# Performance work log

Hardware: AMD Instinct MI355X
Metric: run time of the kernel (lower is better)

The kernel has to match this reference:

```python
import jax, jax.numpy as jnp
import numpy as np

EPS = 0.5
GAM1 = 1.0
GAM2 = 1.0
GAM3 = 1.0
NUM_CLASS = 10


def _logdet(M):
    return jnp.linalg.slogdet(M)[1]


def _discrimn_loss(Z):
    # Z: [n, d] sample-major (original code operates on Z.T of shape (d, n))
    n, d = Z.shape
    scalar = d / (n * EPS)
    I = jnp.eye(d, dtype=Z.dtype)
    return _logdet(I + scalar * (Z.T @ Z)) / 2.0


def _class_grams(Z, Pi):
    # Pi: [n, C] one-hot (float). G[c] = sum_{i in class c} z_i z_i^T  -> [C, d, d]
    return jnp.einsum('nc,nd,ne->cde', Pi, Z, Z)


def _compress_losses(G, counts, d, n):
    # per-class logdet(I + (d/(trPi*eps)) * Gram_c), trPi = count + 1e-8
    C = G.shape[0]
    trPi = counts + 1e-8
    scal = d / (trPi * EPS)                      # [C]
    I = jnp.eye(d, dtype=G.dtype)
    M = I[None, :, :] + scal[:, None, None] * G  # [C, d, d]
    lds = jax.vmap(_logdet)(M)                   # [C]
    lds = jnp.where(counts == 0, 1.0, lds)       # original uses 1.0 for empty class
    scalars = trPi / (2.0 * n)
    return lds, scalars


def setup_inputs() -> dict:
    key = jax.random.key(0)
    k1, k2, k3 = jax.random.split(key, 3)
    n, d = 8192, 512
    Z = jax.random.normal(k1, (n, d), dtype=jnp.float32)
    Z_bar = jax.random.normal(k2, (n, d), dtype=jnp.float32)
    real_label = jax.random.randint(k3, (n,), 0, NUM_CLASS, dtype=jnp.int64 if jax.config.jax_enable_x64 else jnp.int32)
    return {"Z": Z, "Z_bar": Z_bar, "real_label": real_label,
            "ith_inner_loop": 0, "num_inner_loop": 2}


def reference(Z, Z_bar, real_label, ith_inner_loop, num_inner_loop):
    n, d = Z.shape
    Pi = jax.nn.one_hot(real_label, NUM_CLASS, dtype=Z.dtype)  # [n, C]
    counts = Pi.sum(axis=0)                                    # [C]

    # deltaR(Z) and deltaR(Z_bar)
    z_disc = _discrimn_loss(Z)
    zb_disc = _discrimn_loss(Z_bar)
    Gz = _class_grams(Z, Pi)
    Gzb = _class_grams(Z_bar, Pi)
    z_lds, z_scalars = _compress_losses(Gz, counts, d, n)
    zb_lds, zb_scalars = _compress_losses(Gzb, counts, d, n)
    z_comp = jnp.sum(z_scalars * z_lds)
    zb_comp = jnp.sum(zb_scalars * zb_lds)
    z_total = -(z_disc - z_comp)
    zbar_total = -(zb_disc - zb_comp)

    # cross term: for each class j, discrimn loss of cat(Z[y==j], Z_bar[y==j])
    # Gram of concatenation = Gz[j] + Gzb[j]; n_j = 2*count_j
    nj = 2.0 * counts
    scal = d / (nj * EPS)                                       # [C]
    I = jnp.eye(d, dtype=Z.dtype)
    Mcross = I[None, :, :] + scal[:, None, None] * (Gz + Gzb)
    cross_lds = jax.vmap(_logdet)(Mcross) / 2.0
    itemRzjzjbar = jnp.sum(cross_lds)

    errD_ = (GAM1 * (z_disc - z_comp)
             + GAM2 * (zb_disc - zb_comp)
             + GAM3 * (itemRzjzjbar - 0.25 * jnp.sum(z_lds) - 0.25 * jnp.sum(zb_lds)))
    errD = -errD_
    term3 = -itemRzjzjbar + 0.25 * jnp.sum(z_lds) + 0.25 * jnp.sum(zb_lds)
    return (errD, z_total, zbar_total, term3)
```

## Files before the change

### kernel.cpp

```cpp
#include <hip/hip_runtime.h>
#include <math.h>

#define D     512
#define NCLS  10
#define GKB   32
#define NB    16
#define CHOLT 512
#define SSTR  20

__global__ __launch_bounds__(1024) void meta_kernel(const int* __restrict__ labels, int n,
                                                    int* __restrict__ counts,
                                                    int* __restrict__ offsets,
                                                    int* __restrict__ perm) {
    __shared__ int sc[NCLS], scur[NCLS], soff[NCLS + 1];
    int t = threadIdx.x;
    if (t < NCLS) { sc[t] = 0; scur[t] = 0; }
    __syncthreads();
    for (int i = t; i < n; i += 1024) atomicAdd(&sc[labels[i]], 1);
    __syncthreads();
    if (t == 0) {
        int a = 0;
        for (int c = 0; c < NCLS; ++c) { soff[c] = a; a += sc[c]; }
        soff[NCLS] = a;
    }
    __syncthreads();
    for (int i = t; i < n; i += 1024) {
        int l = labels[i];
        int pos = soff[l] + atomicAdd(&scur[l], 1);
        perm[pos] = i;
    }
    if (t < NCLS) { counts[t] = sc[t]; offsets[t] = soff[t]; }
}

__global__ __launch_bounds__(256) void gram_kernel(const float* __restrict__ Z,
                                                   const float* __restrict__ Zb,
                                                   const int* __restrict__ offsets,
                                                   const int* __restrict__ counts,
                                                   const int* __restrict__ perm,
                                                   float* __restrict__ Gz,
                                                   float* __restrict__ Gzb) {
    const int job = blockIdx.y;
    const int tensor = job / NCLS;
    const int c = job % NCLS;
    const float* __restrict__ A = tensor ? Zb : Z;
    float* __restrict__ G = (tensor ? Gzb : Gz) + (size_t)c * D * D;
    const int off = offsets[c], cnt = counts[c];
    const int x0 = (blockIdx.x >> 3) * 128, y0 = (blockIdx.x & 7) * 64;

    __shared__ __align__(16) float As[GKB][128];
    __shared__ __align__(16) float Bs[GKB][64];

    const int t = threadIdx.x;
    const int tx = t & 15, tr = t >> 4;
    float acc[8][4] = {};

    for (int r0 = 0; r0 < cnt; r0 += GKB) {
        #pragma unroll
        for (int it = 0; it < 4; ++it) {
            int q = t + 256 * it;
            int kr = q >> 5, cq = q & 31;
            int r = r0 + kr;
            float4 v = {0.f, 0.f, 0.f, 0.f};
            if (r < cnt) v = *(const float4*)&A[(size_t)perm[off + r] * D + x0 + 4 * cq];
            *(float4*)&As[kr][4 * cq] = v;
        }
        #pragma unroll
        for (int it = 0; it < 2; ++it) {
            int q = t + 256 * it;
            int kr = q >> 4, cq = q & 15;
            int r = r0 + kr;
            float4 v = {0.f, 0.f, 0.f, 0.f};
            if (r < cnt) v = *(const float4*)&A[(size_t)perm[off + r] * D + y0 + 4 * cq];
            *(float4*)&Bs[kr][4 * cq] = v;
        }
        __syncthreads();
        #pragma unroll
        for (int k = 0; k < GKB; ++k) {
            float4 a0 = *(const float4*)&As[k][tr * 8];
            float4 a1 = *(const float4*)&As[k][tr * 8 + 4];
            float4 bb = *(const float4*)&Bs[k][tx * 4];
            float av[8] = {a0.x, a0.y, a0.z, a0.w, a1.x, a1.y, a1.z, a1.w};
            float bv[4] = {bb.x, bb.y, bb.z, bb.w};
            #pragma unroll
            for (int s = 0; s < 8; ++s)
                #pragma unroll
                for (int jj = 0; jj < 4; ++jj)
                    acc[s][jj] = fmaf(av[s], bv[jj], acc[s][jj]);
        }
        __syncthreads();
    }
    #pragma unroll
    for (int s = 0; s < 8; ++s) {
        float4 o = {acc[s][0], acc[s][1], acc[s][2], acc[s][3]};
        *(float4*)&G[(size_t)(x0 + tr * 8 + s) * D + y0 + tx * 4] = o;
    }
}

__global__ __launch_bounds__(256) void gtot_kernel(const float* __restrict__ Gz,
                                                   const float* __restrict__ Gzb,
                                                   float* __restrict__ Tz,
                                                   float* __restrict__ Tzb) {
    const size_t DDv = (size_t)D * D;
    int q = blockIdx.x * 256 + threadIdx.x;
    if (q < 65536) {
        float4 sz = {0.f, 0.f, 0.f, 0.f}, sb = {0.f, 0.f, 0.f, 0.f};
        #pragma unroll
        for (int c = 0; c < NCLS; ++c) {
            float4 a = *(const float4*)&Gz[c * DDv + 4 * (size_t)q];
            float4 b = *(const float4*)&Gzb[c * DDv + 4 * (size_t)q];
            sz.x += a.x; sz.y += a.y; sz.z += a.z; sz.w += a.w;
            sb.x += b.x; sb.y += b.y; sb.z += b.z; sb.w += b.w;
        }
        *(float4*)&Tz[4 * (size_t)q] = sz;
        *(float4*)&Tzb[4 * (size_t)q] = sb;
    }
}

__global__ __launch_bounds__(CHOLT) void chol_kernel(const float* __restrict__ Tz,
                                                     const float* __restrict__ Tzb,
                                                     const float* __restrict__ Gz,
                                                     const float* __restrict__ Gzb,
                                                     const int* __restrict__ counts,
                                                     float* __restrict__ Lout,
                                                     double* __restrict__ logdets, int n) {
    const int m = blockIdx.x;
    const size_t DDv = (size_t)D * D;
    float* __restrict__ A = Lout + (size_t)m * DDv;

    const float* g0; const float* g1 = nullptr;
    double scald;
    if (m == 0)      { g0 = Tz;  scald = (double)D / ((double)n * 0.5); }
    else if (m == 1) { g0 = Tzb; scald = (double)D / ((double)n * 0.5); }
    else if (m < 12) { int c = m - 2;  g0 = Gz  + (size_t)c * DDv;
                       scald = (double)D / (((double)counts[c] + 1e-8) * 0.5); }
    else if (m < 22) { int c = m - 12; g0 = Gzb + (size_t)c * DDv;
                       scald = (double)D / (((double)counts[c] + 1e-8) * 0.5); }
    else             { int c = m - 22; g0 = Gz + (size_t)c * DDv; g1 = Gzb + (size_t)c * DDv;
                       int cnt = counts[c];
                       scald = cnt ? (double)D / ((double)(2 * cnt) * 0.5) : 0.0; }
    const float scal = (float)scald;

    __shared__ __align__(16) float S[2][D * SSTR];
    __shared__ float P[D * (NB + 1)];
    __shared__ float invd[NB];
    __shared__ float diagAll[D];
    __shared__ double wpart[CHOLT / 64];
    const int t = threadIdx.x;
    const int il = t & 127, jg = t >> 7;
    const int srow = t >> 2, skq = (t & 3) * 4;

    for (int b = 0; b < D / NB; ++b) {
        const int J0 = b * NB;
        const int R = D - J0;
        float acc[4][4];
        #pragma unroll
        for (int s2 = 0; s2 < 4; ++s2) {
            int i = il + 128 * s2;
            if (i < R) {
                size_t base = (size_t)(J0 + i) * D + J0 + jg * 4;
                float4 v = *(const float4*)(g0 + base);
                if (g1) {
                    float4 w = *(const float4*)(g1 + base);
                    v.x += w.x; v.y += w.y; v.z += w.z; v.w += w.w;
                }
                float gv[4] = {v.x, v.y, v.z, v.w};
                #pragma unroll
                for (int jj = 0; jj < 4; ++jj)
                    acc[s2][jj] = scal * gv[jj] + ((i == jg * 4 + jj) ? 1.f : 0.f);
            } else {
                #pragma unroll
                for (int jj = 0; jj < 4; ++jj) acc[s2][jj] = 0.f;
            }
        }
        const int nslab = J0 >> 4;
        if (nslab) {
            float4 rg0, rg1, rg2, rg3;
#define SLOAD(kk) { \
            if (srow       < R) rg0 = *(const float4*)&A[(size_t)(J0 + srow      ) * D + (kk) + skq]; \
            if (srow + 128 < R) rg1 = *(const float4*)&A[(size_t)(J0 + srow + 128) * D + (kk) + skq]; \
            if (srow + 256 < R) rg2 = *(const float4*)&A[(size_t)(J0 + srow + 256) * D + (kk) + skq]; \
            if (srow + 384 < R) rg3 = *(const float4*)&A[(size_t)(J0 + srow + 384) * D + (kk) + skq]; }
#define SWRITE(Sb) { \
            if (srow       < R) *(float4*)&(Sb)[(srow      ) * SSTR + skq] = rg0; \
            if (srow + 128 < R) *(float4*)&(Sb)[(srow + 128) * SSTR + skq] = rg1; \
            if (srow + 256 < R) *(float4*)&(Sb)[(srow + 256) * SSTR + skq] = rg2; \
            if (srow + 384 < R) *(float4*)&(Sb)[(srow + 384) * SSTR + skq] = rg3; }
            SLOAD(0); SWRITE(S[0]); __syncthreads();
            int buf = 0;
            for (int ks = 0; ks < nslab; ++ks) {
                const bool more = (ks + 1 < nslab);
                if (more) SLOAD((ks + 1) << 4);
                const float* Sb = &S[buf][0];
                #pragma unroll
                for (int k4 = 0; k4 < 4; ++k4) {
                    float4 bq0 = *(const float4*)&Sb[(jg * 4 + 0) * SSTR + 4 * k4];
                    float4 bq1 = *(const float4*)&Sb[(jg * 4 + 1) * SSTR + 4 * k4];
                    float4 bq2 = *(const float4*)&Sb[(jg * 4 + 2) * SSTR + 4 * k4];
                    float4 bq3 = *(const float4*)&Sb[(jg * 4 + 3) * SSTR + 4 * k4];
                    float bv[4][4] = {{bq0.x, bq0.y, bq0.z, bq0.w},
                                      {bq1.x, bq1.y, bq1.z, bq1.w},
                                      {bq2.x, bq2.y, bq2.z, bq2.w},
                                      {bq3.x, bq3.y, bq3.z, bq3.w}};
                    #pragma unroll
                    for (int s2 = 0; s2 < 4; ++s2) {
                        int i = il + 128 * s2;
                        if (i < R) {
                            float4 aq = *(const float4*)&Sb[i * SSTR + 4 * k4];
                            float av[4] = {aq.x, aq.y, aq.z, aq.w};
                            #pragma unroll
                            for (int jj = 0; jj < 4; ++jj)
                                #pragma unroll
                                for (int u = 0; u < 4; ++u)
                                    acc[s2][jj] = fmaf(-av[u], bv[jj][u], acc[s2][jj]);
                        }
                    }
                }
                if (more) SWRITE(S[buf ^ 1]);
                __syncthreads();
                buf ^= 1;
            }
#undef SLOAD
#undef SWRITE
        }
        __syncthreads();
        #pragma unroll
        for (int s2 = 0; s2 < 4; ++s2) {
            int i = il + 128 * s2;
            if (i < R)
                #pragma unroll
                for (int jj = 0; jj < 4; ++jj)
                    P[i * (NB + 1) + jg * 4 + jj] = acc[s2][jj];
        }
        __syncthreads();
        if (t < NB) {
            float r[NB];
            #pragma unroll
            for (int k = 0; k < NB; ++k) r[k] = P[t * (NB + 1) + k];
            #pragma unroll
            for (int j = 0; j < NB; ++j) {
                float pjj = __shfl(r[j], j, 64);
                float ljj = sqrtf(pjj);
                float inv = 1.0f / ljj;
                if (t == j) r[j] = ljj;
                else if (t > j) r[j] *= inv;
                #pragma unroll
                for (int k2 = j + 1; k2 < NB; ++k2) {
                    float lkj = __shfl(r[j], k2, 64);
                    if (t >= k2) r[k2] -= r[j] * lkj;
                }
            }
            #pragma unroll
            for (int k = 0; k < NB; ++k) P[t * (NB + 1) + k] = r[k];
            diagAll[J0 + t] = r[t];
            invd[t] = 1.0f / r[t];
        }
        __syncthreads();
        {
            int i = NB + t;
            if (i < R) {
                float x[NB];
                #pragma unroll
                for (int k = 0; k < NB; ++k) x[k] = P[i * (NB + 1) + k];
                #pragma unroll
                for (int j = 0; j < NB; ++j) {
                    float tj = x[j];
                    #pragma unroll
                    for (int k = 0; k < NB; ++k)
                        if (k < j) tj -= P[j * (NB + 1) + k] * x[k];
                    x[j] = tj * invd[j];
                }
                #pragma unroll
                for (int k = 0; k < NB; ++k) P[i * (NB + 1) + k] = x[k];
            }
        }
        __syncthreads();
        for (int e = t; e < R * NB; e += CHOLT) {
            int i = e >> 4, j = e & (NB - 1);
            A[(size_t)(J0 + i) * D + J0 + j] = P[i * (NB + 1) + j];
        }
        __syncthreads();
    }
    double part = 0.0;
    for (int i = t; i < D; i += CHOLT) part += log((double)diagAll[i]);
    #pragma unroll
    for (int o = 32; o > 0; o >>= 1) part += __shfl_down(part, o, 64);
    if ((t & 63) == 0) wpart[t >> 6] = part;
    __syncthreads();
    if (t == 0) {
        double s2 = 0.0;
        for (int w = 0; w < CHOLT / 64; ++w) s2 += wpart[w];
        logdets[m] = 2.0 * s2;
    }
}

__global__ void final_kernel(const double* __restrict__ logdets,
                             const int* __restrict__ counts, int n,
                             float* __restrict__ out) {
    if (threadIdx.x == 0 && blockIdx.x == 0) {
        double z_disc  = logdets[0] * 0.5;
        double zb_disc = logdets[1] * 0.5;
        double z_comp = 0.0, zb_comp = 0.0, sum_z = 0.0, sum_zb = 0.0, itemR = 0.0;
        for (int c = 0; c < NCLS; ++c) {
            double cnt = (double)counts[c];
            double zl  = (counts[c] == 0) ? 1.0 : logdets[2 + c];
            double zbl = (counts[c] == 0) ? 1.0 : logdets[12 + c];
            double scal = (cnt + 1e-8) / (2.0 * (double)n);
            z_comp  += scal * zl;
            zb_comp += scal * zbl;
            sum_z   += zl;
            sum_zb  += zbl;
            itemR   += logdets[22 + c] * 0.5;
        }
        double errD_ = (z_disc - z_comp) + (zb_disc - zb_comp)
                     + (itemR - 0.25 * sum_z - 0.25 * sum_zb);
        out[0] = (float)(-errD_);
        out[1] = (float)(-(z_disc - z_comp));
        out[2] = (float)(-(zb_disc - zb_comp));
        out[3] = (float)(-itemR + 0.25 * sum_z + 0.25 * sum_zb);
    }
}

extern "C" void kernel_launch(void* const* d_in, const int* in_sizes, int n_in,
                              void* d_out, int out_size, void* d_ws, size_t ws_size,
                              hipStream_t stream) {
    const float* Z      = (const float*)d_in[0];
    const float* Zb     = (const float*)d_in[1];
    const int*   labels = (const int*)d_in[2];
    const int n = in_sizes[2];
    float* out = (float*)d_out;

    const size_t DDv = (size_t)D * D;
    float*  Gz      = (float*)d_ws;
    float*  Gzb     = Gz + NCLS * DDv;
    float*  Tz      = Gzb + NCLS * DDv;
    float*  Tzb     = Tz + DDv;
    float*  Lout    = Tzb + DDv;
    double* logdets = (double*)(Lout + 32 * DDv);
    int*    counts  = (int*)(logdets + 32);
    int*    offsets = counts + NCLS;
    int*    perm    = offsets + NCLS;

    meta_kernel<<<1, 1024, 0, stream>>>(labels, n, counts, offsets, perm);
    dim3 ggrid(32, 20);
    gram_kernel<<<ggrid, 256, 0, stream>>>(Z, Zb, offsets, counts, perm, Gz, Gzb);
    gtot_kernel<<<256, 256, 0, stream>>>(Gz, Gzb, Tz, Tzb);
    chol_kernel<<<32, CHOLT, 0, stream>>>(Tz, Tzb, Gz, Gzb, counts, Lout, logdets, n);
    final_kernel<<<1, 64, 0, stream>>>(logdets, counts, n, out);
}
```

Baseline: 1.111 ms.

## Split panel update over K across thread groups with shared-memory reduction

The trailing panel update in the blocked Cholesky now gives each of the four thread groups a 4-wide slice of the K dimension for all 16 columns, instead of 4 output columns over the full K. Each thread holds 64 accumulators, and the partial sums are combined through a tree reduction in shared memory. The panel buffer gets a 16-byte-aligned stride of 20 so the triangular solve and write-back can use float4 accesses. This cuts redundant A-row loads from shared memory, at the cost of higher register pressure and extra barriers for the reduction.

New measurement: 956.7 us. 1.16x faster.

```diff
diff --git a/kernel.cpp b/kernel.cpp
--- a/kernel.cpp
+++ b/kernel.cpp
@@ -5,8 +5,8 @@
 #define NCLS  10
 #define GKB   32
 #define NB    16
-#define CHOLT 512
 #define SSTR  20
+#define PSTR  20
 
 __global__ __launch_bounds__(1024) void meta_kernel(const int* __restrict__ labels, int n,
                                                     int* __restrict__ counts,
@@ -116,13 +116,13 @@
     }
 }
 
-__global__ __launch_bounds__(CHOLT) void chol_kernel(const float* __restrict__ Tz,
-                                                     const float* __restrict__ Tzb,
-                                                     const float* __restrict__ Gz,
-                                                     const float* __restrict__ Gzb,
-                                                     const int* __restrict__ counts,
-                                                     float* __restrict__ Lout,
-                                                     double* __restrict__ logdets, int n) {
+__global__ __launch_bounds__(512) void chol_kernel(const float* __restrict__ Tz,
+                                                   const float* __restrict__ Tzb,
+                                                   const float* __restrict__ Gz,
+                                                   const float* __restrict__ Gzb,
+                                                   const int* __restrict__ counts,
+                                                   float* __restrict__ Lout,
+                                                   double* __restrict__ logdets, int n) {
     const int m = blockIdx.x;
     const size_t DDv = (size_t)D * D;
     float* __restrict__ A = Lout + (size_t)m * DDv;
@@ -141,10 +141,10 @@
     const float scal = (float)scald;
 
     __shared__ __align__(16) float S[2][D * SSTR];
-    __shared__ float P[D * (NB + 1)];
+    __shared__ __align__(16) float P[D * PSTR];
     __shared__ float invd[NB];
     __shared__ float diagAll[D];
-    __shared__ double wpart[CHOLT / 64];
+    __shared__ double wpart[8];
     const int t = threadIdx.x;
     const int il = t & 127, jg = t >> 7;
     const int srow = t >> 2, skq = (t & 3) * 4;
@@ -152,24 +152,30 @@
     for (int b = 0; b < D / NB; ++b) {
         const int J0 = b * NB;
         const int R = D - J0;
-        float acc[4][4];
-        #pragma unroll
-        for (int s2 = 0; s2 < 4; ++s2) {
-            int i = il + 128 * s2;
-            if (i < R) {
-                size_t base = (size_t)(J0 + i) * D + J0 + jg * 4;
-                float4 v = *(const float4*)(g0 + base);
-                if (g1) {
-                    float4 w = *(const float4*)(g1 + base);
-                    v.x += w.x; v.y += w.y; v.z += w.z; v.w += w.w;
-                }
-                float gv[4] = {v.x, v.y, v.z, v.w};
-                #pragma unroll
-                for (int jj = 0; jj < 4; ++jj)
-                    acc[s2][jj] = scal * gv[jj] + ((i == jg * 4 + jj) ? 1.f : 0.f);
-            } else {
-                #pragma unroll
-                for (int jj = 0; jj < 4; ++jj) acc[s2][jj] = 0.f;
+        float acc[4][16];
+        #pragma unroll
+        for (int s2 = 0; s2 < 4; ++s2)
+            #pragma unroll
+            for (int j = 0; j < 16; ++j) acc[s2][j] = 0.f;
+        if (jg == 0) {
+            #pragma unroll
+            for (int s2 = 0; s2 < 4; ++s2) {
+                int i = il + 128 * s2;
+                if (i < R) {
+                    size_t base = (size_t)(J0 + i) * D + J0;
+                    #pragma unroll
+                    for (int q = 0; q < 4; ++q) {
+                        float4 v = *(const float4*)(g0 + base + 4 * q);
+                        if (g1) {
+                            float4 w = *(const float4*)(g1 + base + 4 * q);
+                            v.x += w.x; v.y += w.y; v.z += w.z; v.w += w.w;
+                        }
+                        float gv[4] = {v.x, v.y, v.z, v.w};
+                        #pragma unroll
+                        for (int u = 0; u < 4; ++u)
+                            acc[s2][4 * q + u] = scal * gv[u] + ((i == 4 * q + u) ? 1.f : 0.f);
+                    }
+                }
             }
         }
         const int nslab = J0 >> 4;
@@ -191,27 +197,24 @@
                 const bool more = (ks + 1 < nslab);
                 if (more) SLOAD((ks + 1) << 4);
                 const float* Sb = &S[buf][0];
-                #pragma unroll
-                for (int k4 = 0; k4 < 4; ++k4) {
-                    float4 bq0 = *(const float4*)&Sb[(jg * 4 + 0) * SSTR + 4 * k4];
-                    float4 bq1 = *(const float4*)&Sb[(jg * 4 + 1) * SSTR + 4 * k4];
-                    float4 bq2 = *(const float4*)&Sb[(jg * 4 + 2) * SSTR + 4 * k4];
-                    float4 bq3 = *(const float4*)&Sb[(jg * 4 + 3) * SSTR + 4 * k4];
-                    float bv[4][4] = {{bq0.x, bq0.y, bq0.z, bq0.w},
-                                      {bq1.x, bq1.y, bq1.z, bq1.w},
-                                      {bq2.x, bq2.y, bq2.z, bq2.w},
-                                      {bq3.x, bq3.y, bq3.z, bq3.w}};
+                if (il < R) {
+                    float4 bq[16];
+                    #pragma unroll
+                    for (int j = 0; j < 16; ++j)
+                        bq[j] = *(const float4*)&Sb[j * SSTR + jg * 4];
                     #pragma unroll
                     for (int s2 = 0; s2 < 4; ++s2) {
                         int i = il + 128 * s2;
                         if (i < R) {
-                            float4 aq = *(const float4*)&Sb[i * SSTR + 4 * k4];
+                            float4 aq = *(const float4*)&Sb[i * SSTR + jg * 4];
                             float av[4] = {aq.x, aq.y, aq.z, aq.w};
                             #pragma unroll
-                            for (int jj = 0; jj < 4; ++jj)
+                            for (int j = 0; j < 16; ++j) {
+                                float bv[4] = {bq[j].x, bq[j].y, bq[j].z, bq[j].w};
                                 #pragma unroll
                                 for (int u = 0; u < 4; ++u)
-                                    acc[s2][jj] = fmaf(-av[u], bv[jj][u], acc[s2][jj]);
+                                    acc[s2][j] = fmaf(-av[u], bv[u], acc[s2][j]);
+                            }
                         }
                     }
                 }
@@ -222,20 +225,51 @@
 #undef SLOAD
 #undef SWRITE
         }
-        __syncthreads();
-        #pragma unroll
-        for (int s2 = 0; s2 < 4; ++s2) {
-            int i = il + 128 * s2;
-            if (i < R)
-                #pragma unroll
-                for (int jj = 0; jj < 4; ++jj)
-                    P[i * (NB + 1) + jg * 4 + jj] = acc[s2][jj];
-        }
-        __syncthreads();
+        {
+            float* S0 = &S[0][0];
+            float* S1 = &S[1][0];
+#define DUMP(Sx) { \
+            _Pragma("unroll") for (int s2 = 0; s2 < 4; ++s2) { int i = il + 128 * s2; \
+              if (i < R) { _Pragma("unroll") for (int q = 0; q < 4; ++q) { \
+                float4 o = {acc[s2][4*q], acc[s2][4*q+1], acc[s2][4*q+2], acc[s2][4*q+3]}; \
+                *(float4*)&(Sx)[i * SSTR + 4 * q] = o; } } } }
+#define ADDF(Sx) { \
+            _Pragma("unroll") for (int s2 = 0; s2 < 4; ++s2) { int i = il + 128 * s2; \
+              if (i < R) { _Pragma("unroll") for (int q = 0; q < 4; ++q) { \
+                float4 v = *(const float4*)&(Sx)[i * SSTR + 4 * q]; \
+                acc[s2][4*q] += v.x; acc[s2][4*q+1] += v.y; \
+                acc[s2][4*q+2] += v.z; acc[s2][4*q+3] += v.w; } } } }
+            if (jg == 1) DUMP(S0)
+            else if (jg == 3) DUMP(S1)
+            __syncthreads();
+            if (jg == 0) ADDF(S0)
+            else if (jg == 2) ADDF(S1)
+            __syncthreads();
+            if (jg == 2) DUMP(S0)
+            __syncthreads();
+            if (jg == 0) {
+                ADDF(S0)
+                #pragma unroll
+                for (int s2 = 0; s2 < 4; ++s2) {
+                    int i = il + 128 * s2;
+                    if (i < R) {
+                        #pragma unroll
+                        for (int q = 0; q < 4; ++q) {
+                            float4 o = {acc[s2][4*q], acc[s2][4*q+1],
+                                        acc[s2][4*q+2], acc[s2][4*q+3]};
+                            *(float4*)&P[i * PSTR + 4 * q] = o;
+                        }
+                    }
+                }
+            }
+            __syncthreads();
+#undef DUMP
+#undef ADDF
+        }
         if (t < NB) {
             float r[NB];
             #pragma unroll
-            for (int k = 0; k < NB; ++k) r[k] = P[t * (NB + 1) + k];
+            for (int k = 0; k < NB; ++k) r[k] = P[t * PSTR + k];
             #pragma unroll
             for (int j = 0; j < NB; ++j) {
                 float pjj = __shfl(r[j], j, 64);
@@ -250,45 +284,61 @@
                 }
             }
             #pragma unroll
-            for (int k = 0; k < NB; ++k) P[t * (NB + 1) + k] = r[k];
+            for (int k = 0; k < NB; ++k) P[t * PSTR + k] = r[k];
             diagAll[J0 + t] = r[t];
             invd[t] = 1.0f / r[t];
         }
         __syncthreads();
         {
-            int i = NB + t;
-            if (i < R) {
-                float x[NB];
-                #pragma unroll
-                for (int k = 0; k < NB; ++k) x[k] = P[i * (NB + 1) + k];
-                #pragma unroll
-                for (int j = 0; j < NB; ++j) {
+            int i2 = NB + t;
+            if (i2 < R) {
+                float x[16];
+                #pragma unroll
+                for (int q = 0; q < 4; ++q) {
+                    float4 v = *(const float4*)&P[i2 * PSTR + 4 * q];
+                    x[4*q] = v.x; x[4*q+1] = v.y; x[4*q+2] = v.z; x[4*q+3] = v.w;
+                }
+                #pragma unroll
+                for (int j = 0; j < 16; ++j) {
                     float tj = x[j];
                     #pragma unroll
-                    for (int k = 0; k < NB; ++k)
-                        if (k < j) tj -= P[j * (NB + 1) + k] * x[k];
+                    for (int q = 0; q < 4; ++q) {
+                        if (4 * q < j) {
+                            float4 Lv = *(const float4*)&P[j * PSTR + 4 * q];
+                            float Lf[4] = {Lv.x, Lv.y, Lv.z, Lv.w};
+                            #pragma unroll
+                            for (int u = 0; u < 4; ++u)
+                                if (4 * q + u < j) tj -= Lf[u] * x[4 * q + u];
+                        }
+                    }
                     x[j] = tj * invd[j];
                 }
                 #pragma unroll
-                for (int k = 0; k < NB; ++k) P[i * (NB + 1) + k] = x[k];
-            }
-        }
-        __syncthreads();
-        for (int e = t; e < R * NB; e += CHOLT) {
-            int i = e >> 4, j = e & (NB - 1);
-            A[(size_t)(J0 + i) * D + J0 + j] = P[i * (NB + 1) + j];
+                for (int q = 0; q < 4; ++q) {
+                    float4 o = {x[4*q], x[4*q+1], x[4*q+2], x[4*q+3]};
+                    *(float4*)&P[i2 * PSTR + 4 * q] = o;
+                }
+            }
+        }
+        __syncthreads();
+        if (t < R) {
+            #pragma unroll
+            for (int q = 0; q < 4; ++q) {
+                float4 v = *(const float4*)&P[t * PSTR + 4 * q];
+                *(float4*)&A[(size_t)(J0 + t) * D + J0 + 4 * q] = v;
+            }
         }
         __syncthreads();
     }
     double part = 0.0;
-    for (int i = t; i < D; i += CHOLT) part += log((double)diagAll[i]);
+    for (int i = t; i < D; i += 512) part += log((double)diagAll[i]);
     #pragma unroll
     for (int o = 32; o > 0; o >>= 1) part += __shfl_down(part, o, 64);
     if ((t & 63) == 0) wpart[t >> 6] = part;
     __syncthreads();
     if (t == 0) {
         double s2 = 0.0;
-        for (int w = 0; w < CHOLT / 64; ++w) s2 += wpart[w];
+        for (int w = 0; w < 8; ++w) s2 += wpart[w];
         logdets[m] = 2.0 * s2;
     }
 }
@@ -344,6 +394,6 @@
     dim3 ggrid(32, 20);
     gram_kernel<<<ggrid, 256, 0, stream>>>(Z, Zb, offsets, counts, perm, Gz, Gzb);
     gtot_kernel<<<256, 256, 0, stream>>>(Gz, Gzb, Tz, Tzb);
-    chol_kernel<<<32, CHOLT, 0, stream>>>(Tz, Tzb, Gz, Gzb, counts, Lout, logdets, n);
+    chol_kernel<<<32, 512, 0, stream>>>(Tz, Tzb, Gz, Gzb, counts, Lout, logdets, n);
     final_kernel<<<1, 64, 0, stream>>>(logdets, counts, n, out);
 }
```
